# Kernel tuning notes

Hardware: AMD Instinct MI355X
Metric: run time of the kernel (lower is better)

## Reference

```python
import jax, jax.numpy as jnp
import numpy as np

B, N, C_IN, C_OUT, M = 32, 4096, 128, 128, 256


def setup_inputs() -> dict:
    key = jax.random.key(0)
    k1, k2, k3, k4 = jax.random.split(key, 4)
    x = jax.random.normal(k1, (B, N, C_IN), dtype=jnp.float32)
    # Lowest-M eigenvectors of a graph Laplacian are orthonormal columns [N, M];
    # build an equivalent orthonormal basis via QR of a random matrix.
    U, _ = jnp.linalg.qr(jax.random.normal(k2, (N, M), dtype=jnp.float32))
    # complex spectral weights ~ 0.02 * randn (cfloat) split into real/imag parts
    W_real = jax.random.normal(k3, (C_IN, C_OUT, M), dtype=jnp.float32) * 0.02
    W_imag = jax.random.normal(k4, (C_IN, C_OUT, M), dtype=jnp.float32) * 0.02
    return {"x": x, "eigenvectors": U, "W_real": W_real, "W_imag": W_imag}


def reference(x, eigenvectors, W_real, W_imag):
    # Graph Fourier transform: project node features onto spectral modes.
    # x_spec[b, m, c] = sum_n U[n, m] * x[b, n, c]
    x_spec = jnp.einsum('nm,bnc->bmc', eigenvectors, x)  # [B, M, C_in], real
    # Per-mode complex channel mixing, fused into one batched einsum.
    # Original takes .real of (x_spec * W); since x_spec is real,
    # Re(x_spec @ W) = x_spec @ Re(W), so W_imag does not affect the output.
    out_spec_real = jnp.einsum('bmc,com->bmo', x_spec, W_real)  # [B, M, C_out]
    # Inverse graph Fourier transform back to node space.
    return jnp.einsum('nm,bmo->bno', eigenvectors, out_spec_real)  # [B, N, C_out]
```

## Files before the change

### kernel.cpp

```cpp
#include <hip/hip_runtime.h>
#include <hip/hip_bf16.h>

#define BB 32
#define NN 4096
#define CI 128
#define CO 128
#define MM 256
#define KS 8

typedef __hip_bfloat16 bf16;
typedef __attribute__((ext_vector_type(8))) short bf16x8;
typedef __attribute__((ext_vector_type(4))) float f32x4;

__device__ inline void gl_lds16(const void* g, void* l) {
    __builtin_amdgcn_global_load_lds(
        (const __attribute__((address_space(1))) void*)g,
        (__attribute__((address_space(3))) void*)l, 16, 0, 0);
}

__global__ __launch_bounds__(256) void k_cvtU(const float* __restrict__ U,
                                              bf16* __restrict__ Un,
                                              bf16* __restrict__ Ut) {
    const int n0 = blockIdx.x * 64;
    const int m0 = blockIdx.y * 64;
    __shared__ float tile[64][65];
    const int t = threadIdx.x;
    #pragma unroll
    for (int i = 0; i < 16; ++i) {
        int lin = t + i * 256;
        int r = lin >> 6, c = lin & 63;
        float v = U[(n0 + r) * MM + m0 + c];
        tile[r][c] = v;
        Un[(n0 + r) * MM + m0 + c] = __float2bfloat16(v);
    }
    __syncthreads();
    #pragma unroll
    for (int i = 0; i < 16; ++i) {
        int lin = t + i * 256;
        int r = lin >> 6, c = lin & 63;
        Ut[(long)(m0 + r) * NN + n0 + c] = __float2bfloat16(tile[c][r]);
    }
}

__global__ __launch_bounds__(256) void k_trx(const float* __restrict__ x,
                                             bf16* __restrict__ xT) {
    const int c0 = blockIdx.x * 64;
    const int n0 = blockIdx.y * 64;
    const int b  = blockIdx.z;
    __shared__ float tile[64][65];
    const int t = threadIdx.x;
    #pragma unroll
    for (int i = 0; i < 16; ++i) {
        int lin = t + i * 256;
        int r = lin >> 6, c = lin & 63;
        tile[r][c] = x[((long)b * NN + n0 + r) * CI + c0 + c];
    }
    __syncthreads();
    #pragma unroll
    for (int i = 0; i < 16; ++i) {
        int lin = t + i * 256;
        int r = lin >> 6, c = lin & 63;
        xT[((long)b * CI + c0 + r) * NN + n0 + c] = __float2bfloat16(tile[c][r]);
    }
}

__global__ __launch_bounds__(256) void k_wt(const float* __restrict__ W,
                                            bf16* __restrict__ Wt) {
    const int m0 = blockIdx.x * 64;
    const int o0 = blockIdx.y * 64;
    const int c  = blockIdx.z;
    __shared__ float tile[64][65];
    const int t = threadIdx.x;
    #pragma unroll
    for (int i = 0; i < 16; ++i) {
        int lin = t + i * 256;
        int r = lin >> 6, col = lin & 63;
        tile[r][col] = W[((long)c * CO + o0 + r) * MM + m0 + col];
    }
    __syncthreads();
    #pragma unroll
    for (int i = 0; i < 16; ++i) {
        int lin = t + i * 256;
        int r = lin >> 6, col = lin & 63;
        Wt[((long)(m0 + r) * CI + c) * CO + o0 + col] = __float2bfloat16(tile[col][r]);
    }
}

__global__ __launch_bounds__(256) void k_gemm1(const bf16* __restrict__ Ut,
                                               const bf16* __restrict__ xT,
                                               bf16* __restrict__ part) {
    const int ks = blockIdx.x;
    const int m0 = blockIdx.y * 128;
    const int b  = blockIdx.z;
    __shared__ __align__(16) bf16 As[128 * 32];
    __shared__ __align__(16) bf16 Bs[128 * 32];
    const int t    = threadIdx.x;
    const int lane = t & 63;
    const int wave = t >> 6;
    const int wm   = wave >> 1, wn = wave & 1;
    const int fr   = lane & 15;
    const int kg   = (lane >> 4) * 8;
    f32x4 acc[4][4] = {};
    const long xbase = (long)b * CI * NN;
    for (int kt = 0; kt < 512 / 32; ++kt) {
        const int k0 = ks * 512 + kt * 32;
        #pragma unroll
        for (int i = 0; i < 2; ++i) {
            int lin = t + i * 256;
            int r = lin >> 2, kk = (lin & 3) * 8;
            gl_lds16(&Ut[(long)(m0 + r) * NN + k0 + kk], &As[lin * 8]);
            gl_lds16(&xT[xbase + (long)r * NN + k0 + kk], &Bs[lin * 8]);
        }
        __syncthreads();
        bf16x8 a[4], bfr[4];
        #pragma unroll
        for (int i = 0; i < 4; ++i)
            a[i] = *(const bf16x8*)&As[(wm * 64 + i * 16 + fr) * 32 + kg];
        #pragma unroll
        for (int j = 0; j < 4; ++j)
            bfr[j] = *(const bf16x8*)&Bs[(wn * 64 + j * 16 + fr) * 32 + kg];
        #pragma unroll
        for (int i = 0; i < 4; ++i)
            #pragma unroll
            for (int j = 0; j < 4; ++j)
                acc[i][j] = __builtin_amdgcn_mfma_f32_16x16x32_bf16(a[i], bfr[j], acc[i][j], 0, 0, 0);
        __syncthreads();
    }
    const int quad = (lane >> 4) * 4;
    const long pbase = ((long)ks * BB + b) * MM * CI;
    #pragma unroll
    for (int i = 0; i < 4; ++i) {
        #pragma unroll
        for (int j = 0; j < 4; ++j) {
            int mg = m0 + wm * 64 + i * 16 + quad;
            int cg = wn * 64 + j * 16 + fr;
            #pragma unroll
            for (int r = 0; r < 4; ++r)
                part[pbase + (long)(mg + r) * CI + cg] = __float2bfloat16(acc[i][j][r]);
        }
    }
}

__global__ __launch_bounds__(256) void k_mix(const bf16* __restrict__ part,
                                             const bf16* __restrict__ Wt,
                                             bf16* __restrict__ osT) {
    const int blk = blockIdx.x;
    const int mi  = blk >> 1;
    const int m   = (mi & 7) * 32 + (mi >> 3);
    const int o0  = (blk & 1) * 64;
    __shared__ float Wl[CI][64];
    __shared__ float xl[CI][36];
    const int t = threadIdx.x;
    const long wb = (long)m * CI * CO;
    #pragma unroll
    for (int i = 0; i < 4; ++i) {
        int ch = t + i * 256;
        int c = ch >> 3, og = (ch & 7) * 8;
        bf16x8 v = *(const bf16x8*)&Wt[wb + (long)c * CO + o0 + og];
        #pragma unroll
        for (int j = 0; j < 8; ++j) Wl[c][og + j] = __bfloat162float(((const bf16*)&v)[j]);
    }
    #pragma unroll
    for (int i = 0; i < 2; ++i) {
        int ch = t + i * 256;
        int b = ch >> 4, c8 = (ch & 15) * 8;
        float s[8] = {};
        #pragma unroll
        for (int ks = 0; ks < KS; ++ks) {
            bf16x8 v = *(const bf16x8*)&part[(((long)ks * BB + b) * MM + m) * CI + c8];
            #pragma unroll
            for (int j = 0; j < 8; ++j) s[j] += __bfloat162float(((const bf16*)&v)[j]);
        }
        #pragma unroll
        for (int j = 0; j < 8; ++j) xl[c8 + j][b] = s[j];
    }
    __syncthreads();
    const int op = t & 63;
    const int bq = t >> 6;
    float acc[8] = {};
    for (int c = 0; c < CI; ++c) {
        float w = Wl[c][op];
        #pragma unroll
        for (int j = 0; j < 8; ++j)
            acc[j] += xl[c][bq * 8 + j] * w;
    }
    #pragma unroll
    for (int j = 0; j < 8; ++j)
        osT[((long)(bq * 8 + j) * CO + o0 + op) * MM + m] = __float2bfloat16(acc[j]);
}

__global__ __launch_bounds__(256) void k_gemm3(const bf16* __restrict__ Un,
                                               const bf16* __restrict__ osT,
                                               float* __restrict__ out) {
    const int n0 = blockIdx.x * 128;
    const int b  = blockIdx.y;
    __shared__ __align__(16) bf16 As[128 * 32];
    __shared__ __align__(16) bf16 Bs[128 * 32];
    const int t    = threadIdx.x;
    const int lane = t & 63;
    const int wave = t >> 6;
    const int wm   = wave >> 1, wn = wave & 1;
    const int fr   = lane & 15;
    const int kg   = (lane >> 4) * 8;
    f32x4 acc[4][4] = {};
    const long bbase = (long)b * CO * MM;
    for (int kt = 0; kt < MM / 32; ++kt) {
        const int k0 = kt * 32;
        #pragma unroll
        for (int i = 0; i < 2; ++i) {
            int lin = t + i * 256;
            int r = lin >> 2, kk = (lin & 3) * 8;
            gl_lds16(&Un[(long)(n0 + r) * MM + k0 + kk], &As[lin * 8]);
            gl_lds16(&osT[bbase + (long)r * MM + k0 + kk], &Bs[lin * 8]);
        }
        __syncthreads();
        bf16x8 a[4], bfr[4];
        #pragma unroll
        for (int i = 0; i < 4; ++i)
            a[i] = *(const bf16x8*)&As[(wm * 64 + i * 16 + fr) * 32 + kg];
        #pragma unroll
        for (int j = 0; j < 4; ++j)
            bfr[j] = *(const bf16x8*)&Bs[(wn * 64 + j * 16 + fr) * 32 + kg];
        #pragma unroll
        for (int i = 0; i < 4; ++i)
            #pragma unroll
            for (int j = 0; j < 4; ++j)
                acc[i][j] = __builtin_amdgcn_mfma_f32_16x16x32_bf16(a[i], bfr[j], acc[i][j], 0, 0, 0);
        __syncthreads();
    }
    const int quad = (lane >> 4) * 4;
    #pragma unroll
    for (int i = 0; i < 4; ++i) {
        #pragma unroll
        for (int j = 0; j < 4; ++j) {
            int ng = n0 + wm * 64 + i * 16 + quad;
            int og = wn * 64 + j * 16 + fr;
            #pragma unroll
            for (int r = 0; r < 4; ++r)
                out[((long)b * NN + ng + r) * CO + og] = acc[i][j][r];
        }
    }
}

extern "C" void kernel_launch(void* const* d_in, const int* in_sizes, int n_in,
                              void* d_out, int out_size, void* d_ws, size_t ws_size,
                              hipStream_t stream) {
    const float* x  = (const float*)d_in[0];
    const float* U  = (const float*)d_in[1];
    const float* Wr = (const float*)d_in[2];
    float* out = (float*)d_out;

    char* p = (char*)d_ws;
    bf16* xT   = (bf16*)p;  p += (size_t)BB * CI * NN * 2;
    bf16* part = (bf16*)p;  p += (size_t)KS * BB * MM * CI * 2;
    bf16* Ut   = (bf16*)p;  p += (size_t)MM * NN * 2;
    bf16* Un   = (bf16*)p;  p += (size_t)NN * MM * 2;
    bf16* osT  = (bf16*)p;  p += (size_t)BB * CO * MM * 2;
    bf16* Wt   = (bf16*)p;  p += (size_t)MM * CI * CO * 2;

    k_cvtU <<<dim3(NN / 64, MM / 64), 256, 0, stream>>>(U, Un, Ut);
    k_trx  <<<dim3(CI / 64, NN / 64, BB), 256, 0, stream>>>(x, xT);
    k_wt   <<<dim3(MM / 64, CO / 64, CI), 256, 0, stream>>>(Wr, Wt);
    k_gemm1<<<dim3(KS, MM / 128, BB), 256, 0, stream>>>(Ut, xT, part);
    k_mix  <<<dim3(512), 256, 0, stream>>>(part, Wt, osT);
    k_gemm3<<<dim3(NN / 128, BB), 256, 0, stream>>>(Un, osT, out);
}
```

Baseline: 200.7 us.

## Vectorize transpose kernels and widen gemm3 tile across batch columns

The three transpose/convert kernels now use float4 global loads and 16-byte bf16x8 stores instead of scalar accesses, cutting memory transaction counts. The final GEMM treats batch×C_out as one wide column dimension and uses 128x256 tiles, so each block reuses the loaded U tile for two batches and launches half as many blocks. This doubles the accumulator registers per thread (128 floats), which may lower occupancy.

```diff
diff --git a/kernel.cpp b/kernel.cpp
--- a/kernel.cpp
+++ b/kernel.cpp
@@ -35,10 +35,13 @@
     }
     __syncthreads();
     #pragma unroll
-    for (int i = 0; i < 16; ++i) {
-        int lin = t + i * 256;
-        int r = lin >> 6, c = lin & 63;
-        Ut[(long)(m0 + r) * NN + n0 + c] = __float2bfloat16(tile[c][r]);
+    for (int pass = 0; pass < 2; ++pass) {
+        int no = t & 7;
+        int m  = (t >> 3) + pass * 32;
+        bf16 tmp[8];
+        #pragma unroll
+        for (int j = 0; j < 8; ++j) tmp[j] = __float2bfloat16(tile[no * 8 + j][m]);
+        *(bf16x8*)&Ut[(long)(m0 + m) * NN + n0 + no * 8] = *(bf16x8*)tmp;
     }
 }
 
@@ -50,17 +53,22 @@
     __shared__ float tile[64][65];
     const int t = threadIdx.x;
     #pragma unroll
-    for (int i = 0; i < 16; ++i) {
-        int lin = t + i * 256;
-        int r = lin >> 6, c = lin & 63;
-        tile[r][c] = x[((long)b * NN + n0 + r) * CI + c0 + c];
-    }
-    __syncthreads();
-    #pragma unroll
-    for (int i = 0; i < 16; ++i) {
-        int lin = t + i * 256;
-        int r = lin >> 6, c = lin & 63;
-        xT[((long)b * CI + c0 + r) * NN + n0 + c] = __float2bfloat16(tile[c][r]);
+    for (int pass = 0; pass < 4; ++pass) {
+        int r  = (t >> 4) + pass * 16;
+        int c4 = (t & 15) * 4;
+        float4 v = *(const float4*)&x[((long)b * NN + n0 + r) * CI + c0 + c4];
+        tile[r][c4 + 0] = v.x; tile[r][c4 + 1] = v.y;
+        tile[r][c4 + 2] = v.z; tile[r][c4 + 3] = v.w;
+    }
+    __syncthreads();
+    #pragma unroll
+    for (int pass = 0; pass < 2; ++pass) {
+        int no = t & 7;
+        int c  = (t >> 3) + pass * 32;
+        bf16 tmp[8];
+        #pragma unroll
+        for (int j = 0; j < 8; ++j) tmp[j] = __float2bfloat16(tile[no * 8 + j][c]);
+        *(bf16x8*)&xT[((long)b * CI + c0 + c) * NN + n0 + no * 8] = *(bf16x8*)tmp;
     }
 }
 
@@ -72,17 +80,22 @@
     __shared__ float tile[64][65];
     const int t = threadIdx.x;
     #pragma unroll
-    for (int i = 0; i < 16; ++i) {
-        int lin = t + i * 256;
-        int r = lin >> 6, col = lin & 63;
-        tile[r][col] = W[((long)c * CO + o0 + r) * MM + m0 + col];
-    }
-    __syncthreads();
-    #pragma unroll
-    for (int i = 0; i < 16; ++i) {
-        int lin = t + i * 256;
-        int r = lin >> 6, col = lin & 63;
-        Wt[((long)(m0 + r) * CI + c) * CO + o0 + col] = __float2bfloat16(tile[col][r]);
+    for (int pass = 0; pass < 4; ++pass) {
+        int r  = (t >> 4) + pass * 16;
+        int m4 = (t & 15) * 4;
+        float4 v = *(const float4*)&W[((long)c * CO + o0 + r) * MM + m0 + m4];
+        tile[r][m4 + 0] = v.x; tile[r][m4 + 1] = v.y;
+        tile[r][m4 + 2] = v.z; tile[r][m4 + 3] = v.w;
+    }
+    __syncthreads();
+    #pragma unroll
+    for (int pass = 0; pass < 2; ++pass) {
+        int oo = t & 7;
+        int m  = (t >> 3) + pass * 32;
+        bf16 tmp[8];
+        #pragma unroll
+        for (int j = 0; j < 8; ++j) tmp[j] = __float2bfloat16(tile[oo * 8 + j][m]);
+        *(bf16x8*)&Wt[((long)(m0 + m) * CI + c) * CO + o0 + oo * 8] = *(bf16x8*)tmp;
     }
 }
 
@@ -192,18 +205,17 @@
 __global__ __launch_bounds__(256) void k_gemm3(const bf16* __restrict__ Un,
                                                const bf16* __restrict__ osT,
                                                float* __restrict__ out) {
-    const int n0 = blockIdx.x * 128;
-    const int b  = blockIdx.y;
+    const int n0   = blockIdx.x * 128;
+    const int col0 = blockIdx.y * 256;
     __shared__ __align__(16) bf16 As[128 * 32];
-    __shared__ __align__(16) bf16 Bs[128 * 32];
+    __shared__ __align__(16) bf16 Bs[256 * 32];
     const int t    = threadIdx.x;
     const int lane = t & 63;
     const int wave = t >> 6;
     const int wm   = wave >> 1, wn = wave & 1;
     const int fr   = lane & 15;
     const int kg   = (lane >> 4) * 8;
-    f32x4 acc[4][4] = {};
-    const long bbase = (long)b * CO * MM;
+    f32x4 acc[4][8] = {};
     for (int kt = 0; kt < MM / 32; ++kt) {
         const int k0 = kt * 32;
         #pragma unroll
@@ -211,20 +223,25 @@
             int lin = t + i * 256;
             int r = lin >> 2, kk = (lin & 3) * 8;
             gl_lds16(&Un[(long)(n0 + r) * MM + k0 + kk], &As[lin * 8]);
-            gl_lds16(&osT[bbase + (long)r * MM + k0 + kk], &Bs[lin * 8]);
-        }
-        __syncthreads();
-        bf16x8 a[4], bfr[4];
+        }
+        #pragma unroll
+        for (int i = 0; i < 4; ++i) {
+            int lin = t + i * 256;
+            int r = lin >> 2, kk = (lin & 3) * 8;
+            gl_lds16(&osT[(long)(col0 + r) * MM + k0 + kk], &Bs[lin * 8]);
+        }
+        __syncthreads();
+        bf16x8 a[4], bfr[8];
         #pragma unroll
         for (int i = 0; i < 4; ++i)
             a[i] = *(const bf16x8*)&As[(wm * 64 + i * 16 + fr) * 32 + kg];
         #pragma unroll
-        for (int j = 0; j < 4; ++j)
-            bfr[j] = *(const bf16x8*)&Bs[(wn * 64 + j * 16 + fr) * 32 + kg];
-        #pragma unroll
-        for (int i = 0; i < 4; ++i)
-            #pragma unroll
-            for (int j = 0; j < 4; ++j)
+        for (int j = 0; j < 8; ++j)
+            bfr[j] = *(const bf16x8*)&Bs[(wn * 128 + j * 16 + fr) * 32 + kg];
+        #pragma unroll
+        for (int i = 0; i < 4; ++i)
+            #pragma unroll
+            for (int j = 0; j < 8; ++j)
                 acc[i][j] = __builtin_amdgcn_mfma_f32_16x16x32_bf16(a[i], bfr[j], acc[i][j], 0, 0, 0);
         __syncthreads();
     }
@@ -232,12 +249,13 @@
     #pragma unroll
     for (int i = 0; i < 4; ++i) {
         #pragma unroll
-        for (int j = 0; j < 4; ++j) {
-            int ng = n0 + wm * 64 + i * 16 + quad;
-            int og = wn * 64 + j * 16 + fr;
+        for (int j = 0; j < 8; ++j) {
+            int ng  = n0 + wm * 64 + i * 16 + quad;
+            int col = col0 + wn * 128 + j * 16 + fr;
+            int b = col >> 7, o = col & 127;
             #pragma unroll
             for (int r = 0; r < 4; ++r)
-                out[((long)b * NN + ng + r) * CO + og] = acc[i][j][r];
+                out[((long)b * NN + ng + r) * CO + o] = acc[i][j][r];
         }
     }
 }
@@ -263,5 +281,5 @@
     k_wt   <<<dim3(MM / 64, CO / 64, CI), 256, 0, stream>>>(Wr, Wt);
     k_gemm1<<<dim3(KS, MM / 128, BB), 256, 0, stream>>>(Ut, xT, part);
     k_mix  <<<dim3(512), 256, 0, stream>>>(part, Wt, osT);
-    k_gemm3<<<dim3(NN / 128, BB), 256, 0, stream>>>(Un, osT, out);
-}
+    k_gemm3<<<dim3(NN / 128, 16), 256, 0, stream>>>(Un, osT, out);
+}
```

Result: slower. 208.6 us (+3.9%).
